# Optimization experiments

Measured on AMD Instinct MI355X. Metric: run time of the kernel, lower is better.

The kernel has to match this reference:

```python
import jax, jax.numpy as jnp
import numpy as np
import math

DN = ('NCHW', 'OIHW', 'NCHW')

def conv2d(x, w, b=None, pad=0):
    y = jax.lax.conv_general_dilated(x, w, (1, 1), [(pad, pad), (pad, pad)], dimension_numbers=DN)
    if b is not None:
        y = y + b[None, :, None, None]
    return y

def group_norm(x, weight, bias, groups=32, eps=1e-5):
    B, C, H, W = x.shape
    xg = x.reshape(B, groups, C // groups, H, W)
    mean = xg.mean(axis=(2, 3, 4), keepdims=True)
    var = xg.var(axis=(2, 3, 4), keepdims=True)
    xg = (xg - mean) * jax.lax.rsqrt(var + eps)
    return xg.reshape(B, C, H, W) * weight[None, :, None, None] + bias[None, :, None, None]

def swish(x):
    return x * jax.nn.sigmoid(x)

def setup_inputs() -> dict:
    key = jax.random.key(0)
    ks = jax.random.split(key, 20)
    B, C, H, W = 8, 192, 48, 48
    emb = 192
    n_div = 12
    Cq = C // n_div  # 16
    s = 0.02
    return {
        'x': jax.random.normal(ks[0], (B, C, H, W), jnp.float32),
        'xe': jax.random.normal(ks[1], (B, C, H, W), jnp.float32),
        'time_emb': jax.random.normal(ks[2], (B, emb), jnp.float32),
        'gn1_w': jnp.ones((C,), jnp.float32),
        'gn1_b': jnp.zeros((C,), jnp.float32),
        'conv1_w': jax.random.normal(ks[3], (C, C, 3, 3), jnp.float32) * s,
        'conv1_b': jnp.zeros((C,), jnp.float32),
        'aff_w': jax.random.normal(ks[4], (2 * C, emb), jnp.float32) * s,
        'aff_b': jnp.zeros((2 * C,), jnp.float32),
        'gn2_w': jnp.ones((C,), jnp.float32),
        'gn2_b': jnp.zeros((C,), jnp.float32),
        'conv2_w': jax.random.normal(ks[5], (C, C, 3, 3), jnp.float32) * s,
        'conv2_b': jnp.zeros((C,), jnp.float32),
        'q_w': jax.random.normal(ks[6], (Cq, C, 1, 1), jnp.float32) * s,
        'kv_w': jax.random.normal(ks[7], (2 * Cq, C, 1, 1), jnp.float32) * s,
        'out_w': jax.random.normal(ks[8], (C, Cq, 3, 3), jnp.float32) * s,
        'out_b': jnp.zeros((C,), jnp.float32),
    }

def reference(x, xe, time_emb, gn1_w, gn1_b, conv1_w, conv1_b, aff_w, aff_b,
              gn2_w, gn2_b, conv2_w, conv2_b, q_w, kv_w, out_w, out_b):
    B, C, H, W = x.shape
    n_head, n_div = 1, 12
    head_dim = C // (n_head * n_div)

    # ----- ResnetBlock -----
    h = conv2d(swish(group_norm(x, gn1_w, gn1_b)), conv1_w, conv1_b, pad=1)
    # FeatureWiseAffine (use_affine_level=True)
    gb = time_emb @ aff_w.T + aff_b          # [B, 2C]
    gamma, beta = jnp.split(gb, 2, axis=1)   # each [B, C]
    gb_sum = 0.5 * (gamma + beta)[:, :, None, None]
    h = h + gb_sum * h + gb_sum
    h = conv2d(swish(group_norm(h, gn2_w, gn2_b)), conv2_w, conv2_b, pad=1)
    xres = h + x  # res_conv is Identity (dim == dim_out)

    # ----- CrossAttention -----
    Ye, Xe = xe.shape[-2], xe.shape[-1]
    query = conv2d(xres, q_w).reshape(B, n_head, head_dim, H, W)
    kv = conv2d(xe, kv_w).reshape(B, n_head, head_dim * 2, Ye, Xe)
    key_, value = jnp.split(kv, 2, axis=2)
    scale = 1.0 / math.sqrt(C // n_div)
    attn = jnp.einsum('bnchw,bncyx->bnhwyx', query, key_) * scale
    attn = jax.nn.softmax(attn.reshape(B, n_head, H, W, -1), axis=-1)
    attn = attn.reshape(B, n_head, H, W, Ye, Xe)
    out = jnp.einsum('bnhwyx,bncyx->bnchw', attn, value)
    out = conv2d(out.reshape(B, C // n_div, H, W), out_w, out_b, pad=1)
    return out + xres
```

## Files before the change

### kernel.cpp

```cpp
#include <hip/hip_runtime.h>
#include <hip/hip_bf16.h>

#define NB 8
#define NC 192
#define NH 48
#define NW 48
#define NP 2304
#define NGROUPS 32
#define CPG 6
#define NEMB 192
#define NCQ 16

#define PH 50
#define PWS 52
#define ACT_T_ELEMS ((size_t)NB * PH * PWS * NC)
#define AOT_ELEMS   ((size_t)NB * PH * PWS * 16)

typedef __attribute__((ext_vector_type(4))) short s16x4;
typedef __attribute__((ext_vector_type(8))) short s16x8;
typedef __attribute__((ext_vector_type(4))) float f32x4;

static __device__ inline short f2bf(float v) {
  __hip_bfloat16 h = __float2bfloat16(v);
  return *(short*)&h;
}

__global__ __launch_bounds__(256) void wprep_kernel(const float* __restrict__ w,
                                                    short* __restrict__ wbuf) {
  int i = blockIdx.x * 256 + threadIdx.x;
  if (i >= 6 * 9 * 12 * 64 * 8) return;
  int j  = i & 7;
  int l  = (i >> 3) & 63;
  int cf = (i >> 9) % 12;
  int tk = (i >> 9) / 12;
  int t  = tk % 9;
  int kc = tk / 9;
  int co = cf * 16 + (l & 15);
  int ci = kc * 32 + (l >> 4) * 8 + j;
  wbuf[i] = f2bf(w[((size_t)co * NC + ci) * 9 + t]);
}

__global__ __launch_bounds__(256) void wprep_o_kernel(const float* __restrict__ w,
                                                      short* __restrict__ wbuf) {
  int i = blockIdx.x * 256 + threadIdx.x;
  if (i >= 9 * 12 * 64 * 8) return;
  int j  = i & 7;
  int l  = (i >> 3) & 63;
  int cf = (i >> 9) % 12;
  int t  = (i >> 9) / 12;
  int co = cf * 16 + (l & 15);
  int ci = (l >> 4) * 8 + j;
  wbuf[i] = (ci < 16) ? f2bf(w[((size_t)co * 16 + ci) * 9 + t]) : (short)0;
}

__global__ __launch_bounds__(256) void affine_kernel(const float* __restrict__ emb,
                                                     const float* __restrict__ aw,
                                                     const float* __restrict__ ab,
                                                     float* __restrict__ gbsum) {
  int i = blockIdx.x * 256 + threadIdx.x;
  if (i >= NB * NC) return;
  int b = i / NC;
  int c = i - b * NC;
  const float* e  = emb + b * NEMB;
  const float* w0 = aw + c * NEMB;
  const float* w1 = aw + (c + NC) * NEMB;
  float s = 0.f;
  for (int j = 0; j < NEMB; ++j) s += e[j] * (w0[j] + w1[j]);
  gbsum[i] = 0.5f * (s + ab[c] + ab[c + NC]);
}

__global__ __launch_bounds__(256) void halo_zero_kernel(short* __restrict__ actt) {
  int b = blockIdx.y;
  int i = blockIdx.x * 256 + threadIdx.x;
  if (i >= 9600) return;
  int c4 = i % 48;
  int r  = i / 48;
  size_t off;
  if (r < 52)       off = ((size_t)0 * PWS + r) * NC;
  else if (r < 104) off = ((size_t)49 * PWS + (r - 52)) * NC;
  else if (r < 152) off = ((size_t)(r - 104 + 1) * PWS + 0) * NC;
  else              off = ((size_t)(r - 152 + 1) * PWS + 49) * NC;
  *(s16x4*)(&actt[(size_t)b * PH * PWS * NC + off + c4 * 4]) = (s16x4){0, 0, 0, 0};
}

__global__ __launch_bounds__(256) void halo_zero16_kernel(short* __restrict__ aot) {
  int b = blockIdx.x;
  for (int i = threadIdx.x; i < 784; i += 256) {
    int c4  = i & 3;
    int pos = i >> 2;
    int r, col;
    if (pos < 50)       { r = 0;  col = pos; }
    else if (pos < 100) { r = 49; col = pos - 50; }
    else if (pos < 148) { r = pos - 100 + 1; col = 0; }
    else                { r = pos - 148 + 1; col = 49; }
    *(s16x4*)(&aot[(((size_t)b * PH + r) * PWS + col) * 16 + c4 * 4]) = (s16x4){0, 0, 0, 0};
  }
}

__global__ __launch_bounds__(256) void gn_stats_kernel(const float* __restrict__ in,
                                                       float* __restrict__ stats) {
  int bg = blockIdx.x;
  const float4* p = (const float4*)(in + (size_t)bg * (CPG * NP));
  float s = 0.f, s2 = 0.f;
  for (int i = threadIdx.x; i < CPG * NP / 4; i += 256) {
    float4 v = p[i];
    s  += v.x + v.y + v.z + v.w;
    s2 += v.x * v.x + v.y * v.y + v.z * v.z + v.w * v.w;
  }
#pragma unroll
  for (int off = 32; off > 0; off >>= 1) {
    s  += __shfl_down(s, off);
    s2 += __shfl_down(s2, off);
  }
  __shared__ float red[8];
  int wave = threadIdx.x >> 6;
  if ((threadIdx.x & 63) == 0) { red[wave * 2] = s; red[wave * 2 + 1] = s2; }
  __syncthreads();
  if (threadIdx.x == 0) {
    float S  = red[0] + red[2] + red[4] + red[6];
    float S2 = red[1] + red[3] + red[5] + red[7];
    const float invN = 1.f / (float)(CPG * NP);
    float mean = S * invN;
    float var  = S2 * invN - mean * mean;
    stats[bg * 2]     = mean;
    stats[bg * 2 + 1] = rsqrtf(var + 1e-5f);
  }
}

__global__ __launch_bounds__(256) void gn_apply_t_kernel(const float* __restrict__ in,
                                                         const float* __restrict__ stats,
                                                         const float* __restrict__ gw,
                                                         const float* __restrict__ gb,
                                                         short* __restrict__ actt) {
  __shared__ float tile[48 * 193];
  int bh = blockIdx.x;
  int b = bh / NH;
  int h = bh - b * NH;
  int tid = threadIdx.x;
  for (int i = tid; i < 2304; i += 256) {
    int c = i / 12;
    int w = (i % 12) * 4;
    float4 v = *(const float4*)(in + (((size_t)b * NC + c) * NH + h) * NW + w);
    float mean = stats[(b * NGROUPS + c / CPG) * 2];
    float rstd = stats[(b * NGROUPS + c / CPG) * 2 + 1];
    float sc = rstd * gw[c];
    float sh = gb[c] - mean * sc;
    float y;
    y = v.x * sc + sh; tile[(w + 0) * 193 + c] = y / (1.f + __expf(-y));
    y = v.y * sc + sh; tile[(w + 1) * 193 + c] = y / (1.f + __expf(-y));
    y = v.z * sc + sh; tile[(w + 2) * 193 + c] = y / (1.f + __expf(-y));
    y = v.w * sc + sh; tile[(w + 3) * 193 + c] = y / (1.f + __expf(-y));
  }
  __syncthreads();
  short* dst = actt + (((size_t)b * PH + h + 1) * PWS + 1) * NC;
  for (int i = tid; i < 2304; i += 256) {
    int w  = i / 48;
    int c4 = (i - w * 48) * 4;
    s16x4 o;
    o.x = f2bf(tile[w * 193 + c4 + 0]);
    o.y = f2bf(tile[w * 193 + c4 + 1]);
    o.z = f2bf(tile[w * 193 + c4 + 2]);
    o.w = f2bf(tile[w * 193 + c4 + 3]);
    *(s16x4*)(dst + (size_t)w * NC + c4) = o;
  }
}

template <bool AFFINE, bool RESID>
__global__ __launch_bounds__(256) void conv_mfma_kernel(const short* __restrict__ actt,
                                                        const short* __restrict__ wbuf,
                                                        const float* __restrict__ bias,
                                                        const float* __restrict__ gbsum,
                                                        const float* __restrict__ resid,
                                                        float* __restrict__ out) {
  __shared__ short S[4][50][40];
  int bs = blockIdx.x;
  int b = bs / 24;
  int strip = bs - b * 24;
  int coB = blockIdx.y;
  int h0 = strip * 2;
  int tid = threadIdx.x;
  int lane = tid & 63, wave = tid >> 6;
  int wy = wave >> 1, wx = wave & 1;
  int g8 = (lane >> 4) * 8;

  f32x4 acc[2][3];
#pragma unroll
  for (int m = 0; m < 2; ++m)
#pragma unroll
    for (int f = 0; f < 3; ++f) acc[m][f] = (f32x4){0.f, 0.f, 0.f, 0.f};

  const size_t actbase = ((size_t)b * PH + h0) * PWS * NC;

  for (int kc = 0; kc < 6; ++kc) {
    __syncthreads();
    for (int i = tid; i < 800; i += 256) {
      int ci8 = i & 3;
      int rc  = i >> 2;
      int col = rc % 50, r = rc / 50;
      const s16x8* src = (const s16x8*)(actt + actbase + ((size_t)r * PWS + col) * NC +
                                        kc * 32 + ci8 * 8);
      *(s16x8*)(&S[r][col][ci8 * 8]) = *src;
    }
    __syncthreads();
#pragma unroll
    for (int t = 0; t < 9; ++t) {
      int ky = t / 3, kx = t - ky * 3;
      const short* wp = wbuf + ((((size_t)kc * 9 + t) * 12 + (coB * 4 + wy * 2)) * 64 + lane) * 8;
      s16x8 a0 = *(const s16x8*)wp;
      s16x8 a1 = *(const s16x8*)(wp + 64 * 8);
      int row = wx + ky;
#pragma unroll
      for (int f = 0; f < 3; ++f) {
        int col = f * 16 + (lane & 15) + kx;
        s16x8 bf = *(const s16x8*)(&S[row][col][g8]);
        acc[0][f] = __builtin_amdgcn_mfma_f32_16x16x32_bf16(a0, bf, acc[0][f], 0, 0, 0);
        acc[1][f] = __builtin_amdgcn_mfma_f32_16x16x32_bf16(a1, bf, acc[1][f], 0, 0, 0);
      }
    }
  }
  int hout = h0 + wx;
#pragma unroll
  for (int m = 0; m < 2; ++m) {
    int co0 = coB * 64 + wy * 32 + m * 16;
#pragma unroll
    for (int r = 0; r < 4; ++r) {
      int co = co0 + (lane >> 4) * 4 + r;
      float bv = bias[co];
      float s = AFFINE ? gbsum[b * NC + co] : 0.f;
#pragma unroll
      for (int f = 0; f < 3; ++f) {
        int w = f * 16 + (lane & 15);
        size_t o = (((size_t)b * NC + co) * NH + hout) * NW + w;
        float v = acc[m][f][r] + bv;
        if (AFFINE) v = v * (1.f + s) + s;
        if (RESID) v += resid[o];
        out[o] = v;
      }
    }
  }
}

__global__ __launch_bounds__(256) void out_conv_mfma_kernel(const short* __restrict__ aot,
                                                            const short* __restrict__ wbuf,
                                                            const float* __restrict__ bias,
                                                            float* __restrict__ out) {
  __shared__ short S[4][50][40];
  int bs = blockIdx.x;
  int b = bs / 24;
  int strip = bs - b * 24;
  int coB = blockIdx.y;
  int h0 = strip * 2;
  int tid = threadIdx.x;
  int lane = tid & 63, wave = tid >> 6;
  int wy = wave >> 1, wx = wave & 1;
  int g8 = (lane >> 4) * 8;

  f32x4 acc[2][3];
#pragma unroll
  for (int m = 0; m < 2; ++m)
#pragma unroll
    for (int f = 0; f < 3; ++f) acc[m][f] = (f32x4){0.f, 0.f, 0.f, 0.f};

  const size_t base = ((size_t)b * PH + h0) * PWS * 16;
  for (int i = tid; i < 800; i += 256) {
    int ci8 = i & 3;
    int rc  = i >> 2;
    int col = rc % 50, r = rc / 50;
    s16x8 v = (s16x8){0, 0, 0, 0, 0, 0, 0, 0};
    if (ci8 < 2)
      v = *(const s16x8*)(aot + base + ((size_t)r * PWS + col) * 16 + ci8 * 8);
    *(s16x8*)(&S[r][col][ci8 * 8]) = v;
  }
  __syncthreads();
#pragma unroll
  for (int t = 0; t < 9; ++t) {
    int ky = t / 3, kx = t - ky * 3;
    const short* wp = wbuf + (((size_t)t * 12 + (coB * 4 + wy * 2)) * 64 + lane) * 8;
    s16x8 a0 = *(const s16x8*)wp;
    s16x8 a1 = *(const s16x8*)(wp + 64 * 8);
    int row = wx + ky;
#pragma unroll
    for (int f = 0; f < 3; ++f) {
      int col = f * 16 + (lane & 15) + kx;
      s16x8 bf = *(const s16x8*)(&S[row][col][g8]);
      acc[0][f] = __builtin_amdgcn_mfma_f32_16x16x32_bf16(a0, bf, acc[0][f], 0, 0, 0);
      acc[1][f] = __builtin_amdgcn_mfma_f32_16x16x32_bf16(a1, bf, acc[1][f], 0, 0, 0);
    }
  }
  int hout = h0 + wx;
#pragma unroll
  for (int m = 0; m < 2; ++m) {
    int co0 = coB * 64 + wy * 32 + m * 16;
#pragma unroll
    for (int r = 0; r < 4; ++r) {
      int co = co0 + (lane >> 4) * 4 + r;
      float bv = bias[co];
#pragma unroll
      for (int f = 0; f < 3; ++f) {
        int w = f * 16 + (lane & 15);
        size_t o = (((size_t)b * NC + co) * NH + hout) * NW + w;
        out[o] = acc[m][f][r] + bv + out[o];
      }
    }
  }
}

template <int NOUT>
__global__ __launch_bounds__(256) void prep_partial_kernel(const float* __restrict__ X,
                                                           const float* __restrict__ W,
                                                           float* __restrict__ part) {
  __shared__ float wl[NOUT][64];
  int pt = blockIdx.x, ch = blockIdx.y, b = blockIdx.z;
  for (int i = threadIdx.x; i < NOUT * 64; i += 256) {
    int o = i >> 6, c = i & 63;
    wl[o][c] = W[o * NC + ch * 64 + c];
  }
  __syncthreads();
  int p = pt * 256 + threadIdx.x;
  const float* ip = X + ((size_t)b * NC + ch * 64) * NP + p;
  float acc[NOUT];
#pragma unroll
  for (int o = 0; o < NOUT; ++o) acc[o] = 0.f;
#pragma unroll 8
  for (int ci = 0; ci < 64; ++ci) {
    float xv = ip[(size_t)ci * NP];
#pragma unroll
    for (int o = 0; o < NOUT; ++o) acc[o] += xv * wl[o][ci];
  }
  float* op = part + ((size_t)(ch * NB + b) * NOUT) * NP + p;
#pragma unroll
  for (int o = 0; o < NOUT; ++o) op[(size_t)o * NP] = acc[o];
}

__global__ __launch_bounds__(256) void prep_pack_kernel(const float* __restrict__ pq,
                                                        const float* __restrict__ pkv,
                                                        short* __restrict__ Qb,
                                                        short* __restrict__ Kb,
                                                        short* __restrict__ VTb) {
  __shared__ short QL[16][264], KL[16][264];
  int pt = blockIdx.x, b = blockIdx.y;
  int tp = threadIdx.x;
  int p  = pt * 256 + tp;
  const float SC = 0.36067376022224085f;
#pragma unroll
  for (int o = 0; o < 16; ++o) {
    float s = pq[((size_t)(0 * NB + b) * 16 + o) * NP + p] +
              pq[((size_t)(1 * NB + b) * 16 + o) * NP + p] +
              pq[((size_t)(2 * NB + b) * 16 + o) * NP + p];
    QL[o][tp] = f2bf(s * SC);
  }
#pragma unroll
  for (int o = 0; o < 32; ++o) {
    float s = pkv[((size_t)(0 * NB + b) * 32 + o) * NP + p] +
              pkv[((size_t)(1 * NB + b) * 32 + o) * NP + p] +
              pkv[((size_t)(2 * NB + b) * 32 + o) * NP + p];
    if (o < 16) KL[o][tp] = f2bf(s);
    else VTb[((size_t)b * 16 + (o - 16)) * NP + p] = f2bf(s);
  }
  __syncthreads();
  short* qp = Qb + ((size_t)b * NP + p) * 32;
  short* kp = Kb + ((size_t)b * NP + p) * 32;
#pragma unroll
  for (int o4 = 0; o4 < 4; ++o4) {
    s16x4 vq = {QL[o4 * 4 + 0][tp], QL[o4 * 4 + 1][tp], QL[o4 * 4 + 2][tp], QL[o4 * 4 + 3][tp]};
    s16x4 vk = {KL[o4 * 4 + 0][tp], KL[o4 * 4 + 1][tp], KL[o4 * 4 + 2][tp], KL[o4 * 4 + 3][tp]};
    *(s16x4*)(qp + o4 * 4) = vq;
    *(s16x4*)(kp + o4 * 4) = vk;
    *(s16x4*)(qp + 16 + o4 * 4) = (s16x4){0, 0, 0, 0};
    *(s16x4*)(kp + 16 + o4 * 4) = (s16x4){0, 0, 0, 0};
  }
}

__global__ __launch_bounds__(256) void attn_mfma_kernel(const short* __restrict__ Qb,
                                                        const short* __restrict__ Kb,
                                                        const short* __restrict__ VTb,
                                                        short* __restrict__ aot) {
  int b    = blockIdx.y;
  int lane = threadIdx.x & 63;
  int wave = threadIdx.x >> 6;
  int q0   = (blockIdx.x * 4 + wave) * 16;
  int g    = lane >> 4;
  int ql   = lane & 15;

  s16x8 qfrag = *(const s16x8*)(Qb + ((size_t)b * NP + q0 + ql) * 32 + g * 8);

  int r0 = 8 * (ql >> 2) + (ql & 3);
  const short* Kbase = Kb + (size_t)b * NP * 32 + g * 8;
  const short* Vbase = VTb + ((size_t)b * 16 + ql) * NP;

  f32x4 acc = {0.f, 0.f, 0.f, 0.f};
  float m = -1e30f, l = 0.f;

  s16x8 kf0 = *(const s16x8*)(Kbase + (size_t)r0 * 32);
  s16x8 kf1 = *(const s16x8*)(Kbase + (size_t)(r0 + 4) * 32);
  s16x8 vf  = *(const s16x8*)(Vbase + g * 8);

  for (int step = 0; step < 72; ++step) {
    int k0n = (step < 71) ? (step + 1) * 32 : 0;
    s16x8 nk0 = *(const s16x8*)(Kbase + (size_t)(k0n + r0) * 32);
    s16x8 nk1 = *(const s16x8*)(Kbase + (size_t)(k0n + r0 + 4) * 32);
    s16x8 nv  = *(const s16x8*)(Vbase + k0n + g * 8);

    f32x4 z = {0.f, 0.f, 0.f, 0.f};
    f32x4 s0 = __builtin_amdgcn_mfma_f32_16x16x32_bf16(kf0, qfrag, z, 0, 0, 0);
    f32x4 s1 = __builtin_amdgcn_mfma_f32_16x16x32_bf16(kf1, qfrag, z, 0, 0, 0);

    float tm = fmaxf(fmaxf(fmaxf(s0[0], s0[1]), fmaxf(s0[2], s0[3])),
                     fmaxf(fmaxf(s1[0], s1[1]), fmaxf(s1[2], s1[3])));
    tm = fmaxf(tm, __shfl_xor(tm, 16, 64));
    tm = fmaxf(tm, __shfl_xor(tm, 32, 64));
    float mn = fmaxf(m, tm);
    float corr = exp2f(m - mn);
    m = mn;
    float p0 = exp2f(s0[0] - m), p1 = exp2f(s0[1] - m);
    float p2 = exp2f(s0[2] - m), p3 = exp2f(s0[3] - m);
    float p4 = exp2f(s1[0] - m), p5 = exp2f(s1[1] - m);
    float p6 = exp2f(s1[2] - m), p7 = exp2f(s1[3] - m);
    l = l * corr + ((p0 + p1) + (p2 + p3)) + ((p4 + p5) + (p6 + p7));
    acc[0] *= corr; acc[1] *= corr; acc[2] *= corr; acc[3] *= corr;

    s16x8 pf;
    pf[0] = f2bf(p0); pf[1] = f2bf(p1); pf[2] = f2bf(p2); pf[3] = f2bf(p3);
    pf[4] = f2bf(p4); pf[5] = f2bf(p5); pf[6] = f2bf(p6); pf[7] = f2bf(p7);
    acc = __builtin_amdgcn_mfma_f32_16x16x32_bf16(vf, pf, acc, 0, 0, 0);

    kf0 = nk0; kf1 = nk1; vf = nv;
  }
  l += __shfl_xor(l, 16, 64);
  l += __shfl_xor(l, 32, 64);
  float inv = 1.f / l;
  int q = q0 + ql;
  int h = q / NW, w = q - h * NW;
  s16x4 o;
  o.x = f2bf(acc[0] * inv);
  o.y = f2bf(acc[1] * inv);
  o.z = f2bf(acc[2] * inv);
  o.w = f2bf(acc[3] * inv);
  *(s16x4*)(aot + (((size_t)b * PH + h + 1) * PWS + w + 1) * 16 + g * 4) = o;
}

extern "C" void kernel_launch(void* const* d_in, const int* in_sizes, int n_in,
                              void* d_out, int out_size, void* d_ws, size_t ws_size,
                              hipStream_t stream) {
  const float* x      = (const float*)d_in[0];
  const float* xe     = (const float*)d_in[1];
  const float* temb   = (const float*)d_in[2];
  const float* gn1w   = (const float*)d_in[3];
  const float* gn1b   = (const float*)d_in[4];
  const float* conv1w = (const float*)d_in[5];
  const float* conv1b = (const float*)d_in[6];
  const float* affw   = (const float*)d_in[7];
  const float* affb   = (const float*)d_in[8];
  const float* gn2w   = (const float*)d_in[9];
  const float* gn2b   = (const float*)d_in[10];
  const float* conv2w = (const float*)d_in[11];
  const float* conv2b = (const float*)d_in[12];
  const float* qw     = (const float*)d_in[13];
  const float* kvw    = (const float*)d_in[14];
  const float* outw   = (const float*)d_in[15];
  const float* outb   = (const float*)d_in[16];
  float* out = (float*)d_out;
  float* ws  = (float*)d_ws;

  float* gbsum  = ws;
  float* stats  = gbsum + NB * NC;
  float* partQ  = stats + 512;
  float* partKV = partQ + (size_t)3 * NB * 16 * NP;
  short* wbuf1  = (short*)(partKV + (size_t)3 * NB * 32 * NP);
  short* wbuf2  = wbuf1 + (size_t)6 * 9 * 12 * 64 * 8;
  short* wbufo  = wbuf2 + (size_t)6 * 9 * 12 * 64 * 8;
  short* actt   = wbufo + (size_t)9 * 12 * 64 * 8;
  short* Qb     = actt + ACT_T_ELEMS;
  short* Kb     = Qb + (size_t)NB * NP * 32;
  short* VTb    = Kb + (size_t)NB * NP * 32;
  short* aot    = VTb + (size_t)NB * 16 * NP;

  wprep_kernel<<<1296, 256, 0, stream>>>(conv1w, wbuf1);
  wprep_kernel<<<1296, 256, 0, stream>>>(conv2w, wbuf2);
  wprep_o_kernel<<<216, 256, 0, stream>>>(outw, wbufo);
  affine_kernel<<<6, 256, 0, stream>>>(temb, affw, affb, gbsum);
  halo_zero_kernel<<<dim3(38, NB), 256, 0, stream>>>(actt);
  halo_zero16_kernel<<<NB, 256, 0, stream>>>(aot);
  prep_partial_kernel<32><<<dim3(9, 3, NB), 256, 0, stream>>>(xe, kvw, partKV);

  gn_stats_kernel<<<NB * NGROUPS, 256, 0, stream>>>(x, stats);
  gn_apply_t_kernel<<<NB * NH, 256, 0, stream>>>(x, stats, gn1w, gn1b, actt);
  conv_mfma_kernel<true, false><<<dim3(NB * 24, 3), 256, 0, stream>>>(
      actt, wbuf1, conv1b, gbsum, nullptr, out);
  gn_stats_kernel<<<NB * NGROUPS, 256, 0, stream>>>(out, stats);
  gn_apply_t_kernel<<<NB * NH, 256, 0, stream>>>(out, stats, gn2w, gn2b, actt);
  conv_mfma_kernel<false, true><<<dim3(NB * 24, 3), 256, 0, stream>>>(
      actt, wbuf2, conv2b, nullptr, x, out);

  prep_partial_kernel<16><<<dim3(9, 3, NB), 256, 0, stream>>>(out, qw, partQ);
  prep_pack_kernel<<<dim3(9, NB), 256, 0, stream>>>(partQ, partKV, Qb, Kb, VTb);
  attn_mfma_kernel<<<dim3(36, NB), 256, 0, stream>>>(Qb, Kb, VTb, aot);
  out_conv_mfma_kernel<<<dim3(NB * 24, 3), 256, 0, stream>>>(aot, wbufo, outb, out);
}
```

Before: 308.3 us.

## Split attention key range across four waves and merge softmax partials in LDS

```diff
diff --git a/kernel.cpp b/kernel.cpp
--- a/kernel.cpp
+++ b/kernel.cpp
@@ -371,14 +371,18 @@
   }
 }
 
-__global__ __launch_bounds__(256) void attn_mfma_kernel(const short* __restrict__ Qb,
-                                                        const short* __restrict__ Kb,
-                                                        const short* __restrict__ VTb,
-                                                        short* __restrict__ aot) {
+__global__ __launch_bounds__(1024) void attn_mfma_kernel(const short* __restrict__ Qb,
+                                                         const short* __restrict__ Kb,
+                                                         const short* __restrict__ VTb,
+                                                         short* __restrict__ aot) {
+  __shared__ float PM[4][4][64], PL[4][4][64];
+  __shared__ f32x4 PA[4][4][64];
   int b    = blockIdx.y;
-  int lane = threadIdx.x & 63;
-  int wave = threadIdx.x >> 6;
-  int q0   = (blockIdx.x * 4 + wave) * 16;
+  int tid  = threadIdx.x;
+  int lane = tid & 63;
+  int w    = tid >> 6;
+  int qg   = w & 3, ks = w >> 2;
+  int q0   = blockIdx.x * 64 + qg * 16;
   int g    = lane >> 4;
   int ql   = lane & 15;
 
@@ -391,15 +395,16 @@
   f32x4 acc = {0.f, 0.f, 0.f, 0.f};
   float m = -1e30f, l = 0.f;
 
-  s16x8 kf0 = *(const s16x8*)(Kbase + (size_t)r0 * 32);
-  s16x8 kf1 = *(const s16x8*)(Kbase + (size_t)(r0 + 4) * 32);
-  s16x8 vf  = *(const s16x8*)(Vbase + g * 8);
-
-  for (int step = 0; step < 72; ++step) {
-    int k0n = (step < 71) ? (step + 1) * 32 : 0;
-    s16x8 nk0 = *(const s16x8*)(Kbase + (size_t)(k0n + r0) * 32);
-    s16x8 nk1 = *(const s16x8*)(Kbase + (size_t)(k0n + r0 + 4) * 32);
-    s16x8 nv  = *(const s16x8*)(Vbase + k0n + g * 8);
+  int kk = ks * 576;
+  s16x8 kf0 = *(const s16x8*)(Kbase + (size_t)(kk + r0) * 32);
+  s16x8 kf1 = *(const s16x8*)(Kbase + (size_t)(kk + r0 + 4) * 32);
+  s16x8 vf  = *(const s16x8*)(Vbase + kk + g * 8);
+
+  for (int step = 0; step < 18; ++step) {
+    int kn = (step < 17) ? kk + 32 : ks * 576;
+    s16x8 nk0 = *(const s16x8*)(Kbase + (size_t)(kn + r0) * 32);
+    s16x8 nk1 = *(const s16x8*)(Kbase + (size_t)(kn + r0 + 4) * 32);
+    s16x8 nv  = *(const s16x8*)(Vbase + kn + g * 8);
 
     f32x4 z = {0.f, 0.f, 0.f, 0.f};
     f32x4 s0 = __builtin_amdgcn_mfma_f32_16x16x32_bf16(kf0, qfrag, z, 0, 0, 0);
@@ -407,36 +412,57 @@
 
     float tm = fmaxf(fmaxf(fmaxf(s0[0], s0[1]), fmaxf(s0[2], s0[3])),
                      fmaxf(fmaxf(s1[0], s1[1]), fmaxf(s1[2], s1[3])));
-    tm = fmaxf(tm, __shfl_xor(tm, 16, 64));
-    tm = fmaxf(tm, __shfl_xor(tm, 32, 64));
-    float mn = fmaxf(m, tm);
-    float corr = exp2f(m - mn);
-    m = mn;
+    if (!__all(tm <= m + 8.0f)) {
+      tm = fmaxf(tm, __shfl_xor(tm, 16, 64));
+      tm = fmaxf(tm, __shfl_xor(tm, 32, 64));
+      float mn = fmaxf(m, tm);
+      float corr = exp2f(m - mn);
+      m = mn;
+      l *= corr;
+      acc[0] *= corr; acc[1] *= corr; acc[2] *= corr; acc[3] *= corr;
+    }
     float p0 = exp2f(s0[0] - m), p1 = exp2f(s0[1] - m);
     float p2 = exp2f(s0[2] - m), p3 = exp2f(s0[3] - m);
     float p4 = exp2f(s1[0] - m), p5 = exp2f(s1[1] - m);
     float p6 = exp2f(s1[2] - m), p7 = exp2f(s1[3] - m);
-    l = l * corr + ((p0 + p1) + (p2 + p3)) + ((p4 + p5) + (p6 + p7));
-    acc[0] *= corr; acc[1] *= corr; acc[2] *= corr; acc[3] *= corr;
+    l += ((p0 + p1) + (p2 + p3)) + ((p4 + p5) + (p6 + p7));
 
     s16x8 pf;
     pf[0] = f2bf(p0); pf[1] = f2bf(p1); pf[2] = f2bf(p2); pf[3] = f2bf(p3);
     pf[4] = f2bf(p4); pf[5] = f2bf(p5); pf[6] = f2bf(p6); pf[7] = f2bf(p7);
     acc = __builtin_amdgcn_mfma_f32_16x16x32_bf16(vf, pf, acc, 0, 0, 0);
 
-    kf0 = nk0; kf1 = nk1; vf = nv;
-  }
-  l += __shfl_xor(l, 16, 64);
-  l += __shfl_xor(l, 32, 64);
-  float inv = 1.f / l;
-  int q = q0 + ql;
-  int h = q / NW, w = q - h * NW;
-  s16x4 o;
-  o.x = f2bf(acc[0] * inv);
-  o.y = f2bf(acc[1] * inv);
-  o.z = f2bf(acc[2] * inv);
-  o.w = f2bf(acc[3] * inv);
-  *(s16x4*)(aot + (((size_t)b * PH + h + 1) * PWS + w + 1) * 16 + g * 4) = o;
+    kf0 = nk0; kf1 = nk1; vf = nv; kk = kn;
+  }
+  PM[ks][qg][lane] = m;
+  PL[ks][qg][lane] = l;
+  PA[ks][qg][lane] = acc;
+  __syncthreads();
+  if (ks == 0) {
+    float M = PM[0][qg][lane];
+#pragma unroll
+    for (int k = 1; k < 4; ++k) M = fmaxf(M, PM[k][qg][lane]);
+    float L = 0.f;
+    f32x4 o = {0.f, 0.f, 0.f, 0.f};
+#pragma unroll
+    for (int k = 0; k < 4; ++k) {
+      float c = exp2f(PM[k][qg][lane] - M);
+      L += PL[k][qg][lane] * c;
+      f32x4 a = PA[k][qg][lane];
+      o[0] += a[0] * c; o[1] += a[1] * c; o[2] += a[2] * c; o[3] += a[3] * c;
+    }
+    L += __shfl_xor(L, 16, 64);
+    L += __shfl_xor(L, 32, 64);
+    float inv = 1.f / L;
+    int q = q0 + ql;
+    int h = q / NW, wcol = q - h * NW;
+    s16x4 ov;
+    ov.x = f2bf(o[0] * inv);
+    ov.y = f2bf(o[1] * inv);
+    ov.z = f2bf(o[2] * inv);
+    ov.w = f2bf(o[3] * inv);
+    *(s16x4*)(aot + (((size_t)b * PH + h + 1) * PWS + wcol + 1) * 16 + g * 4) = ov;
+  }
 }
 
 extern "C" void kernel_launch(void* const* d_in, const int* in_sizes, int n_in,
@@ -494,6 +520,6 @@
 
   prep_partial_kernel<16><<<dim3(9, 3, NB), 256, 0, stream>>>(out, qw, partQ);
   prep_pack_kernel<<<dim3(9, NB), 256, 0, stream>>>(partQ, partKV, Qb, Kb, VTb);
-  attn_mfma_kernel<<<dim3(36, NB), 256, 0, stream>>>(Qb, Kb, VTb, aot);
+  attn_mfma_kernel<<<dim3(36, NB), 1024, 0, stream>>>(Qb, Kb, VTb, aot);
   out_conv_mfma_kernel<<<dim3(NB * 24, 3), 256, 0, stream>>>(aot, wbufo, outb, out);
 }
```

After: 300.8 us. -2.4%, faster.
